# Kernel optimization log

Measured on AMD Instinct MI355X. Metric: run time of the kernel, lower is better.

Reference implementation:

```python
import jax, jax.numpy as jnp
import numpy as np

NEG_INF = -1e18  # fp32 masking constant used by the original module


def setup_inputs() -> dict:
    key0 = jax.random.key(0)
    kq, kk, kv, km, ke = jax.random.split(key0, 5)
    B, L, H, C = 2, 2048, 16, 64
    query = jax.random.normal(kq, (B, L, H, C), dtype=jnp.float32)
    key = jax.random.normal(kk, (B, L, H, C), dtype=jnp.float32)
    value = jax.random.normal(kv, (B, L, H, C), dtype=jnp.float32)
    mask = jax.random.randint(km, (B, L, L), 0, 2).astype(jnp.bool_)
    edge_scores = jax.random.normal(ke, (1, H, L, L), dtype=jnp.float32)
    return {"query": query, "key": key, "value": value, "mask": mask,
            "edge_scores": edge_scores}


def _masked_softmax(att_score, mask):
    # mask: True -> keep, False -> masked. Fill with -1e18 (fp32 path),
    # softmax, then multiply by mask (post-softmax zeroing), as in original.
    s = jnp.where(mask, att_score, NEG_INF)
    w = jax.nn.softmax(s, axis=-1)
    return w * mask.astype(w.dtype)


def reference(query, key, value, mask, edge_scores):
    # layout 'NTK': query/key/value (B, L, H, C); mask (B, Lq, Lm)
    scale = jnp.sqrt(jnp.asarray(query.shape[-1], dtype=query.dtype))
    # scores: (B, H, Lq, Lm)
    scores = jnp.einsum('binc,bjnc->bnij', query, key)
    scores = scores + edge_scores
    attn_weights = _masked_softmax(scores / scale, mask[:, None, :, :])
    # dropout rate is 0.0 -> identity
    # context: (B, Lq, H, Cv) -> (B, Lq, H*Cv)
    context = jnp.einsum('bnij,bjnc->binc', attn_weights, value)
    B, Lq = context.shape[0], context.shape[1]
    context_vec = context.reshape(B, Lq, -1)
    return (context_vec, scores, attn_weights)
```

## Files before the change

kernel.cpp:

```cpp
#include <hip/hip_runtime.h>


typedef __attribute__((ext_vector_type(8))) short bf16x8;
typedef __attribute__((ext_vector_type(4))) float f32x4;
typedef __attribute__((ext_vector_type(4))) int   i32x4;

#define LQ 2048
#define NH 16
#define CD 64

__device__ inline short f2bf(float x) {
    union { float f; unsigned u; } v; v.f = x;
    unsigned r = v.u + 0x7FFFu + ((v.u >> 16) & 1u);
    return (short)(r >> 16);
}

__device__ inline bf16x8 pack8(f32x4 a, f32x4 b) {
    bf16x8 r;
    r[0] = f2bf(a[0]); r[1] = f2bf(a[1]); r[2] = f2bf(a[2]); r[3] = f2bf(a[3]);
    r[4] = f2bf(b[0]); r[5] = f2bf(b[1]); r[6] = f2bf(b[2]); r[7] = f2bf(b[3]);
    return r;
}

__global__ __launch_bounds__(256, 3)
void k_main(const float* __restrict__ q, const float* __restrict__ kk,
            const float* __restrict__ v, const int* __restrict__ mask,
            const float* __restrict__ edge,
            float* __restrict__ sc, float* __restrict__ attn,
            float* __restrict__ ctx, float* __restrict__ invout)
{
    __shared__ short Ks[64][72];
    __shared__ short Vt[64][72];
    __shared__ short Wt[4][16][72];

    const int z = blockIdx.y;
    const int b = z & 1, h = z >> 1;
    const int i0 = blockIdx.x * 64;
    const int tid = threadIdx.x;
    const int r = tid >> 2, seg = (tid & 3) * 16;
    const int wave = tid >> 6, lane = tid & 63;
    const int quad = lane >> 4, mm = lane & 15;

    const int gi = i0 + wave * 16 + mm;
    const float* qp = q + ((size_t)((b * LQ + gi) * NH + h)) * CD;
    bf16x8 qa0 = pack8(*(const f32x4*)(qp + quad * 8), *(const f32x4*)(qp + quad * 8 + 4));
    bf16x8 qa1 = pack8(*(const f32x4*)(qp + 32 + quad * 8), *(const f32x4*)(qp + 32 + quad * 8 + 4));

    const float* erow = edge + ((size_t)(h * LQ + gi)) * LQ;
    const int*   mrow = mask + ((size_t)(b * LQ + gi)) * LQ;
    const size_t srow = ((size_t)((b * NH + h) * LQ + gi)) * LQ;

    f32x4 ev[4]; i32x4 mv[4];
    #pragma unroll
    for (int jt = 0; jt < 4; ++jt) {
        ev[jt] = __builtin_nontemporal_load((const f32x4*)(erow + jt * 16 + quad * 4));
        mv[jt] = *(const i32x4*)(mrow + jt * 16 + quad * 4);
    }
    f32x4 kr[4], vr[4];
    {
        const float* kp = kk + ((size_t)((b * LQ + r) * NH + h)) * CD + seg;
        const float* vp = v  + ((size_t)((b * LQ + r) * NH + h)) * CD + seg;
        #pragma unroll
        for (int u = 0; u < 4; ++u) { kr[u] = ((const f32x4*)kp)[u]; vr[u] = ((const f32x4*)vp)[u]; }
    }

    float lacc = 0.f;
    f32x4 cacc[4] = { {0,0,0,0}, {0,0,0,0}, {0,0,0,0}, {0,0,0,0} };

    for (int jb = 0; jb < 32; ++jb) {
        const int j0 = jb * 64;
        __syncthreads();
        #pragma unroll
        for (int u = 0; u < 4; ++u) {
            *(short4*)&Ks[r][seg + u * 4] =
                make_short4(f2bf(kr[u][0]), f2bf(kr[u][1]), f2bf(kr[u][2]), f2bf(kr[u][3]));
            Vt[seg + u * 4 + 0][r] = f2bf(vr[u][0]);
            Vt[seg + u * 4 + 1][r] = f2bf(vr[u][1]);
            Vt[seg + u * 4 + 2][r] = f2bf(vr[u][2]);
            Vt[seg + u * 4 + 3][r] = f2bf(vr[u][3]);
        }
        if (jb < 31) {
            const float* kp = kk + ((size_t)((b * LQ + j0 + 64 + r) * NH + h)) * CD + seg;
            const float* vp = v  + ((size_t)((b * LQ + j0 + 64 + r) * NH + h)) * CD + seg;
            #pragma unroll
            for (int u = 0; u < 4; ++u) { kr[u] = ((const f32x4*)kp)[u]; vr[u] = ((const f32x4*)vp)[u]; }
        }
        __syncthreads();

        f32x4 acc[4];
        #pragma unroll
        for (int jt = 0; jt < 4; ++jt) {
            bf16x8 k0 = *(const bf16x8*)&Ks[jt * 16 + mm][quad * 8];
            bf16x8 k1 = *(const bf16x8*)&Ks[jt * 16 + mm][32 + quad * 8];
            f32x4 a = {0.f, 0.f, 0.f, 0.f};
            a = __builtin_amdgcn_mfma_f32_16x16x32_bf16(k0, qa0, a, 0, 0, 0);
            a = __builtin_amdgcn_mfma_f32_16x16x32_bf16(k1, qa1, a, 0, 0, 0);
            acc[jt] = a;
        }

        #pragma unroll
        for (int jt = 0; jt < 4; ++jt) {
            const int jl = jt * 16 + quad * 4;
            f32x4 s4 = acc[jt] + ev[jt];
            __builtin_nontemporal_store(s4, (f32x4*)(sc + srow + j0 + jl));
            f32x4 p;
            p[0] = mv[jt][0] ? __expf(s4[0] * 0.125f) : 0.f;
            p[1] = mv[jt][1] ? __expf(s4[1] * 0.125f) : 0.f;
            p[2] = mv[jt][2] ? __expf(s4[2] * 0.125f) : 0.f;
            p[3] = mv[jt][3] ? __expf(s4[3] * 0.125f) : 0.f;
            __builtin_nontemporal_store(p, (f32x4*)(attn + srow + j0 + jl));
            *(short4*)&Wt[wave][mm][jl] = make_short4(f2bf(p[0]), f2bf(p[1]), f2bf(p[2]), f2bf(p[3]));
            lacc += (p[0] + p[1]) + (p[2] + p[3]);
        }

        if (jb < 31) {
            #pragma unroll
            for (int jt = 0; jt < 4; ++jt) {
                ev[jt] = __builtin_nontemporal_load((const f32x4*)(erow + j0 + 64 + jt * 16 + quad * 4));
                mv[jt] = *(const i32x4*)(mrow + j0 + 64 + jt * 16 + quad * 4);
            }
        }

        #pragma unroll
        for (int kt = 0; kt < 2; ++kt) {
            bf16x8 aw = *(const bf16x8*)&Wt[wave][mm][kt * 32 + quad * 8];
            #pragma unroll
            for (int nt = 0; nt < 4; ++nt) {
                bf16x8 bb = *(const bf16x8*)&Vt[nt * 16 + mm][kt * 32 + quad * 8];
                cacc[nt] = __builtin_amdgcn_mfma_f32_16x16x32_bf16(aw, bb, cacc[nt], 0, 0, 0);
            }
        }
    }

    lacc += __shfl_xor(lacc, 16, 64);
    lacc += __shfl_xor(lacc, 32, 64);
    const float inv = (lacc > 0.f) ? 1.f / lacc : 0.f;
    if (quad == 0)
        invout[(size_t)(b * NH + h) * LQ + gi] = inv;

    float inv4[4];
    #pragma unroll
    for (int reg = 0; reg < 4; ++reg)
        inv4[reg] = __shfl(inv, quad * 4 + reg, 64);

    const int irow = i0 + wave * 16 + quad * 4;
    #pragma unroll
    for (int nt = 0; nt < 4; ++nt) {
        const int c = nt * 16 + mm;
        #pragma unroll
        for (int reg = 0; reg < 4; ++reg) {
            const int i = irow + reg;
            __builtin_nontemporal_store(cacc[nt][reg] * inv4[reg],
                                        ctx + ((size_t)(b * LQ + i)) * (NH * CD) + h * CD + c);
        }
    }
}

__global__ __launch_bounds__(256)
void k_norm(float* __restrict__ attn, const float* __restrict__ inv)
{
    const size_t total4 = (size_t)2 * NH * LQ * LQ / 4;
    size_t idx = (size_t)blockIdx.x * 256 + threadIdx.x;
    const size_t stride = (size_t)gridDim.x * 256;
    for (; idx < total4; idx += stride) {
        const float iv = inv[(idx * 4) >> 11];
        f32x4 w = __builtin_nontemporal_load((const f32x4*)attn + idx);
        w *= iv;
        __builtin_nontemporal_store(w, (f32x4*)attn + idx);
    }
}

extern "C" void kernel_launch(void* const* d_in, const int* in_sizes, int n_in,
                              void* d_out, int out_size, void* d_ws, size_t ws_size,
                              hipStream_t stream) {
    const float* q    = (const float*)d_in[0];
    const float* k    = (const float*)d_in[1];
    const float* v    = (const float*)d_in[2];
    const int*   mask = (const int*)d_in[3];
    const float* edge = (const float*)d_in[4];

    float* out = (float*)d_out;
    float* ctx = out;
    float* sc  = out + 4194304;
    float* at  = sc + 134217728;

    float* inv = (float*)d_ws;

    k_main<<<dim3(32, 32), 256, 0, stream>>>(q, k, v, mask, edge, sc, at, ctx, inv);
    k_norm<<<dim3(2048), 256, 0, stream>>>(at, inv);
}
```

Measured before the change: 1.718 ms.

## Drop K/V register prefetch, raise occupancy bound, use plain loads/stores

Removes the register-staged prefetch of the next K/V tile and loads K/V directly before converting them into shared memory. This frees registers, and the launch bound is raised from 3 to 4 blocks per SM. It also swaps nontemporal loads and stores for ordinary ones on edge, scores, attn and ctx. The trade is less latency hiding for K/V loads and possibly more cache pollution from the large streaming outputs.

```diff
diff --git a/kernel.cpp b/kernel.cpp
--- a/kernel.cpp
+++ b/kernel.cpp
@@ -22,7 +22,7 @@
     return r;
 }
 
-__global__ __launch_bounds__(256, 3)
+__global__ __launch_bounds__(256, 4)
 void k_main(const float* __restrict__ q, const float* __restrict__ kk,
             const float* __restrict__ v, const int* __restrict__ mask,
             const float* __restrict__ edge,
@@ -53,15 +53,8 @@
     f32x4 ev[4]; i32x4 mv[4];
     #pragma unroll
     for (int jt = 0; jt < 4; ++jt) {
-        ev[jt] = __builtin_nontemporal_load((const f32x4*)(erow + jt * 16 + quad * 4));
+        ev[jt] = *(const f32x4*)(erow + jt * 16 + quad * 4);
         mv[jt] = *(const i32x4*)(mrow + jt * 16 + quad * 4);
-    }
-    f32x4 kr[4], vr[4];
-    {
-        const float* kp = kk + ((size_t)((b * LQ + r) * NH + h)) * CD + seg;
-        const float* vp = v  + ((size_t)((b * LQ + r) * NH + h)) * CD + seg;
-        #pragma unroll
-        for (int u = 0; u < 4; ++u) { kr[u] = ((const f32x4*)kp)[u]; vr[u] = ((const f32x4*)vp)[u]; }
     }
 
     float lacc = 0.f;
@@ -70,20 +63,17 @@
     for (int jb = 0; jb < 32; ++jb) {
         const int j0 = jb * 64;
         __syncthreads();
+        const float* krow = kk + ((size_t)((b * LQ + j0 + r) * NH + h)) * CD + seg;
+        const float* vrow = v  + ((size_t)((b * LQ + j0 + r) * NH + h)) * CD + seg;
         #pragma unroll
         for (int u = 0; u < 4; ++u) {
-            *(short4*)&Ks[r][seg + u * 4] =
-                make_short4(f2bf(kr[u][0]), f2bf(kr[u][1]), f2bf(kr[u][2]), f2bf(kr[u][3]));
-            Vt[seg + u * 4 + 0][r] = f2bf(vr[u][0]);
-            Vt[seg + u * 4 + 1][r] = f2bf(vr[u][1]);
-            Vt[seg + u * 4 + 2][r] = f2bf(vr[u][2]);
-            Vt[seg + u * 4 + 3][r] = f2bf(vr[u][3]);
-        }
-        if (jb < 31) {
-            const float* kp = kk + ((size_t)((b * LQ + j0 + 64 + r) * NH + h)) * CD + seg;
-            const float* vp = v  + ((size_t)((b * LQ + j0 + 64 + r) * NH + h)) * CD + seg;
-            #pragma unroll
-            for (int u = 0; u < 4; ++u) { kr[u] = ((const f32x4*)kp)[u]; vr[u] = ((const f32x4*)vp)[u]; }
+            f32x4 g = ((const f32x4*)krow)[u];
+            *(short4*)&Ks[r][seg + u * 4] = make_short4(f2bf(g[0]), f2bf(g[1]), f2bf(g[2]), f2bf(g[3]));
+            f32x4 w = ((const f32x4*)vrow)[u];
+            Vt[seg + u * 4 + 0][r] = f2bf(w[0]);
+            Vt[seg + u * 4 + 1][r] = f2bf(w[1]);
+            Vt[seg + u * 4 + 2][r] = f2bf(w[2]);
+            Vt[seg + u * 4 + 3][r] = f2bf(w[3]);
         }
         __syncthreads();
 
@@ -102,13 +92,13 @@
         for (int jt = 0; jt < 4; ++jt) {
             const int jl = jt * 16 + quad * 4;
             f32x4 s4 = acc[jt] + ev[jt];
-            __builtin_nontemporal_store(s4, (f32x4*)(sc + srow + j0 + jl));
+            *(f32x4*)(sc + srow + j0 + jl) = s4;
             f32x4 p;
             p[0] = mv[jt][0] ? __expf(s4[0] * 0.125f) : 0.f;
             p[1] = mv[jt][1] ? __expf(s4[1] * 0.125f) : 0.f;
             p[2] = mv[jt][2] ? __expf(s4[2] * 0.125f) : 0.f;
             p[3] = mv[jt][3] ? __expf(s4[3] * 0.125f) : 0.f;
-            __builtin_nontemporal_store(p, (f32x4*)(attn + srow + j0 + jl));
+            *(f32x4*)(attn + srow + j0 + jl) = p;
             *(short4*)&Wt[wave][mm][jl] = make_short4(f2bf(p[0]), f2bf(p[1]), f2bf(p[2]), f2bf(p[3]));
             lacc += (p[0] + p[1]) + (p[2] + p[3]);
         }
@@ -116,7 +106,7 @@
         if (jb < 31) {
             #pragma unroll
             for (int jt = 0; jt < 4; ++jt) {
-                ev[jt] = __builtin_nontemporal_load((const f32x4*)(erow + j0 + 64 + jt * 16 + quad * 4));
+                ev[jt] = *(const f32x4*)(erow + j0 + 64 + jt * 16 + quad * 4);
                 mv[jt] = *(const i32x4*)(mrow + j0 + 64 + jt * 16 + quad * 4);
             }
         }
@@ -150,8 +140,7 @@
         #pragma unroll
         for (int reg = 0; reg < 4; ++reg) {
             const int i = irow + reg;
-            __builtin_nontemporal_store(cacc[nt][reg] * inv4[reg],
-                                        ctx + ((size_t)(b * LQ + i)) * (NH * CD) + h * CD + c);
+            ctx[((size_t)(b * LQ + i)) * (NH * CD) + h * CD + c] = cacc[nt][reg] * inv4[reg];
         }
     }
 }
```

After: 1.716 ms. Within noise of the previous version (-0.1%).
